# Performance work log

Measured on AMD Instinct MI355X. Metric: run time of the kernel, lower is better.

## Reference

```python
import jax, jax.numpy as jnp
import numpy as np

NQ, M, ND, N, H, DIM = 32, 32, 200, 160, 768, 128
TEMP = 0.1      # log_softmax temperature
TAU = 0.5       # gumbel-softmax temperature
NEG = -10000.0


def _l2norm(x):
    # F.normalize(p=2, dim=-1) with eps clamp
    n = jnp.maximum(jnp.linalg.norm(x, axis=-1, keepdims=True), 1e-12)
    return x / n


def setup_inputs() -> dict:
    key = jax.random.key(0)
    k1, k2, k3, k4, k5, k6 = jax.random.split(key, 6)
    Q = jax.random.normal(k1, (NQ, M, H), dtype=jnp.float32)
    D = jax.random.normal(k2, (ND, N, H), dtype=jnp.float32)
    q_mask = jax.random.randint(k3, (NQ, M), 0, 2).astype(jnp.float32)
    d_mask = jax.random.randint(k4, (ND, N), 0, 2).astype(jnp.float32)
    # pre-sampled Gumbel(0,1) noise for gumbel_softmax (fixed for determinism)
    u = jax.random.uniform(k5, (NQ, ND, M, N), dtype=jnp.float32,
                           minval=1e-6, maxval=1.0 - 1e-6)
    gumbel_noise = -jnp.log(-jnp.log(u))
    # proj_linear: Linear(768, dim, bias=False)
    W_proj = jax.random.normal(k6, (H, DIM), dtype=jnp.float32) / np.sqrt(H)
    return {"Q": Q, "D": D, "q_mask": q_mask, "d_mask": d_mask,
            "gumbel_noise": gumbel_noise, "W_proj": W_proj}


def reference(Q, D, q_mask, d_mask, gumbel_noise, W_proj):
    # project + L2-normalize token embeddings
    Qp = _l2norm(Q @ W_proj)            # [q, m, dim]
    Dp = _l2norm(D @ W_proj)            # [d, n, dim]

    # pairwise token similarities: [q, d, m, n]
    sim = jnp.einsum('qmh,dnh->qdmn', Qp, Dp)

    dm = d_mask[None, :, None, :]       # [1, d, 1, n]
    sim_masked = sim * dm + (1.0 - dm) * NEG

    logits = jax.nn.log_softmax(sim_masked / TEMP, axis=-1)

    # gumbel_softmax(tau=0.5, hard=True) with straight-through
    y_soft = jax.nn.softmax((logits + gumbel_noise) / TAU, axis=-1)
    idx = jnp.argmax(y_soft, axis=-1)
    y_hard = jax.nn.one_hot(idx, N, dtype=y_soft.dtype)
    y = jax.lax.stop_gradient(y_hard - y_soft) + y_soft

    # select doc token per query token, mask query tokens, sum -> [q, d]
    scores = (y * sim_masked).sum(-1)          # [q, d, m]
    scores = scores * q_mask[:, None, :]
    return scores.sum(-1)                      # [q, d]
```

## Files before the change

kernel.cpp:

```cpp
#include <hip/hip_runtime.h>
#include <math.h>

#define NQ_   32
#define M_    32
#define ND_   200
#define N_    160
#define H_    768
#define DIM_  128

__global__ __launch_bounds__(128) void proj_norm_row_kernel(
    const float* __restrict__ X, const float* __restrict__ W,
    float* __restrict__ Y)
{
    const int row = blockIdx.x;
    const int c   = threadIdx.x;
    const float* x = X + (size_t)row * H_;
    float acc = 0.0f;
#pragma unroll 8
    for (int h = 0; h < H_; ++h)
        acc = fmaf(x[h], W[(size_t)h * DIM_ + c], acc);

    float ss = __fmul_rn(acc, acc);
    ss = __fadd_rn(ss, __shfl_xor(ss, 1));
    ss = __fadd_rn(ss, __shfl_xor(ss, 2));
    ss = __fadd_rn(ss, __shfl_xor(ss, 4));
    ss = __fadd_rn(ss, __shfl_xor(ss, 8));
    ss = __fadd_rn(ss, __shfl_xor(ss, 16));
    ss = __fadd_rn(ss, __shfl_xor(ss, 32));
    __shared__ float sred[2];
    if ((c & 63) == 0) sred[c >> 6] = ss;
    __syncthreads();
    float tot = __fadd_rn(sred[0], sred[1]);
    float nrm = fmaxf(sqrtf(tot), 1e-12f);
    Y[(size_t)row * DIM_ + c] = acc / nrm;
}

__global__ __launch_bounds__(256) void proj_norm_tiled_kernel(
    const float* __restrict__ X, const float* __restrict__ W,
    float* __restrict__ Y)
{
    __shared__ float Xt[16][128];
    __shared__ float Ws[16][128];
    const int tid = threadIdx.x;
    const int rb  = blockIdx.x * 128;
    const int cg  = tid & 15;
    const int rg  = tid >> 4;

    float acc[8][8];
#pragma unroll
    for (int i = 0; i < 8; ++i)
#pragma unroll
        for (int j = 0; j < 8; ++j) acc[i][j] = 0.0f;

    for (int kc = 0; kc < H_; kc += 16) {
#pragma unroll
        for (int it = 0; it < 2; ++it) {
            int f = tid + it * 256;
            int row = f >> 2;
            int c4  = f & 3;
            float4 v = *reinterpret_cast<const float4*>(
                &X[(size_t)(rb + row) * H_ + kc + c4 * 4]);
            Xt[c4*4+0][row] = v.x;
            Xt[c4*4+1][row] = v.y;
            Xt[c4*4+2][row] = v.z;
            Xt[c4*4+3][row] = v.w;
        }
#pragma unroll
        for (int it = 0; it < 2; ++it) {
            int f = tid + it * 256;
            int wr = f >> 5;
            int wc = f & 31;
            float4 v = *reinterpret_cast<const float4*>(
                &W[(size_t)(kc + wr) * DIM_ + wc * 4]);
            *reinterpret_cast<float4*>(&Ws[wr][wc * 4]) = v;
        }
        __syncthreads();
#pragma unroll
        for (int k = 0; k < 16; ++k) {
            float a[8], b[8];
            *reinterpret_cast<float4*>(&a[0]) = *reinterpret_cast<const float4*>(&Xt[k][rg*8]);
            *reinterpret_cast<float4*>(&a[4]) = *reinterpret_cast<const float4*>(&Xt[k][rg*8+4]);
            *reinterpret_cast<float4*>(&b[0]) = *reinterpret_cast<const float4*>(&Ws[k][cg*8]);
            *reinterpret_cast<float4*>(&b[4]) = *reinterpret_cast<const float4*>(&Ws[k][cg*8+4]);
#pragma unroll
            for (int i = 0; i < 8; ++i)
#pragma unroll
                for (int j = 0; j < 8; ++j)
                    acc[i][j] = fmaf(a[i], b[j], acc[i][j]);
        }
        __syncthreads();
    }

#pragma unroll
    for (int i = 0; i < 8; ++i) {
        float ss = 0.0f;
#pragma unroll
        for (int j = 0; j < 8; ++j) ss = __fadd_rn(ss, __fmul_rn(acc[i][j], acc[i][j]));
        ss = __fadd_rn(ss, __shfl_xor(ss, 1));
        ss = __fadd_rn(ss, __shfl_xor(ss, 2));
        ss = __fadd_rn(ss, __shfl_xor(ss, 4));
        ss = __fadd_rn(ss, __shfl_xor(ss, 8));
        float nrm = fmaxf(sqrtf(ss), 1e-12f);
        float o[8];
#pragma unroll
        for (int j = 0; j < 8; ++j) o[j] = acc[i][j] / nrm;
        size_t base = (size_t)(rb + rg*8 + i) * DIM_ + cg*8;
        *reinterpret_cast<float4*>(&Y[base])     = *reinterpret_cast<float4*>(&o[0]);
        *reinterpret_cast<float4*>(&Y[base + 4]) = *reinterpret_cast<float4*>(&o[4]);
    }
}

__global__ __launch_bounds__(256) void score_kernel(
    const float* __restrict__ Qp, const float* __restrict__ Dp,
    const float* __restrict__ qmask, const float* __restrict__ dmask,
    const float* __restrict__ gum, float* __restrict__ out)
{
    __shared__ float Qt[16][32];
    __shared__ float Dt[4][16][164];
    const int tid  = threadIdx.x;
    const int w    = tid >> 6;
    const int lane = tid & 63;
    const int mg   = lane >> 4;
    const int ng   = lane & 15;
    const int q    = blockIdx.x & 31;
    const int db   = blockIdx.x >> 5;
    const int d    = db * 4 + w;

    const float* Qb = Qp + (size_t)q * M_ * DIM_;
    const float* Db = Dp + (size_t)d * N_ * DIM_;

    float acc[8][10];
#pragma unroll
    for (int i = 0; i < 8; ++i)
#pragma unroll
        for (int j = 0; j < 10; ++j) acc[i][j] = 0.0f;

    for (int kc = 0; kc < DIM_; kc += 16) {
        if (tid < 128) {
            int m = tid >> 2, c4 = tid & 3;
            float4 v = *reinterpret_cast<const float4*>(&Qb[(size_t)m * DIM_ + kc + c4*4]);
            Qt[c4*4+0][m] = v.x;
            Qt[c4*4+1][m] = v.y;
            Qt[c4*4+2][m] = v.z;
            Qt[c4*4+3][m] = v.w;
        }
#pragma unroll
        for (int it = 0; it < 10; ++it) {
            int f = lane + it * 64;
            int n = f >> 2, c4 = f & 3;
            float4 v = *reinterpret_cast<const float4*>(&Db[(size_t)n * DIM_ + kc + c4*4]);
            Dt[w][c4*4+0][n] = v.x;
            Dt[w][c4*4+1][n] = v.y;
            Dt[w][c4*4+2][n] = v.z;
            Dt[w][c4*4+3][n] = v.w;
        }
        __syncthreads();
#pragma unroll
        for (int k = 0; k < 16; ++k) {
            float a[8], b[10];
            *reinterpret_cast<float4*>(&a[0]) = *reinterpret_cast<const float4*>(&Qt[k][mg*8]);
            *reinterpret_cast<float4*>(&a[4]) = *reinterpret_cast<const float4*>(&Qt[k][mg*8+4]);
            const float* bp = &Dt[w][k][ng*10];
#pragma unroll
            for (int j2 = 0; j2 < 5; ++j2)
                *reinterpret_cast<float2*>(&b[j2*2]) = *reinterpret_cast<const float2*>(&bp[j2*2]);
#pragma unroll
            for (int i = 0; i < 8; ++i)
#pragma unroll
                for (int j = 0; j < 10; ++j)
                    acc[i][j] = fmaf(a[i], b[j], acc[i][j]);
        }
        __syncthreads();
    }

    float dmv[10];
#pragma unroll
    for (int j = 0; j < 10; ++j)
        dmv[j] = dmask[(size_t)d * N_ + ng*10 + j];

    const float* gq = gum + ((size_t)q * ND_ + d) * ((size_t)M_ * N_);

    float partial = 0.0f;
#pragma unroll
    for (int i = 0; i < 8; ++i) {
        const int m = mg*8 + i;
        float x[10];
        float mx = -3.402823466e38f;
#pragma unroll
        for (int j = 0; j < 10; ++j) {
            float sm = (dmv[j] != 0.0f) ? acc[i][j] : -10000.0f;
            x[j] = sm / 0.1f;
            mx = fmaxf(mx, x[j]);
        }
        mx = fmaxf(mx, __shfl_xor(mx, 1));
        mx = fmaxf(mx, __shfl_xor(mx, 2));
        mx = fmaxf(mx, __shfl_xor(mx, 4));
        mx = fmaxf(mx, __shfl_xor(mx, 8));

        float se = 0.0f;
#pragma unroll
        for (int j = 0; j < 10; ++j) se = __fadd_rn(se, expf(x[j] - mx));
        se = __fadd_rn(se, __shfl_xor(se, 1));
        se = __fadd_rn(se, __shfl_xor(se, 2));
        se = __fadd_rn(se, __shfl_xor(se, 4));
        se = __fadd_rn(se, __shfl_xor(se, 8));
        const float lse = logf(se);

        float g[10];
        const float2* gp = reinterpret_cast<const float2*>(&gq[(size_t)m * N_ + ng*10]);
#pragma unroll
        for (int j2 = 0; j2 < 5; ++j2)
            *reinterpret_cast<float2*>(&g[j2*2]) = gp[j2];

        float z[10];
        float mz = -3.402823466e38f;
#pragma unroll
        for (int j = 0; j < 10; ++j) {
            z[j] = ((x[j] - mx - lse) + g[j]) / 0.5f;
            mz = fmaxf(mz, z[j]);
        }
        mz = fmaxf(mz, __shfl_xor(mz, 1));
        mz = fmaxf(mz, __shfl_xor(mz, 2));
        mz = fmaxf(mz, __shfl_xor(mz, 4));
        mz = fmaxf(mz, __shfl_xor(mz, 8));

        float e2[10];
        float s2 = 0.0f;
#pragma unroll
        for (int j = 0; j < 10; ++j) { e2[j] = expf(z[j] - mz); s2 = __fadd_rn(s2, e2[j]); }
        s2 = __fadd_rn(s2, __shfl_xor(s2, 1));
        s2 = __fadd_rn(s2, __shfl_xor(s2, 2));
        s2 = __fadd_rn(s2, __shfl_xor(s2, 4));
        s2 = __fadd_rn(s2, __shfl_xor(s2, 8));

        float besty = -1.0f; int bestn = 0x7fffffff; float bests = 0.0f;
#pragma unroll
        for (int j = 0; j < 10; ++j) {
            float y = e2[j] / s2;
            if (y > besty) {
                besty = y;
                bestn = ng*10 + j;
                bests = (dmv[j] != 0.0f) ? acc[i][j] : -10000.0f;
            }
        }
#pragma unroll
        for (int dl = 1; dl < 16; dl <<= 1) {
            float oy = __shfl_xor(besty, dl);
            int   on = __shfl_xor(bestn, dl);
            float os = __shfl_xor(bests, dl);
            if (oy > besty || (oy == besty && on < bestn)) {
                besty = oy; bestn = on; bests = os;
            }
        }
        const float qmv = qmask[q * M_ + m];
        if (ng == 0) partial = __fadd_rn(partial, __fmul_rn(bests, qmv));
    }
    partial = __fadd_rn(partial, __shfl_xor(partial, 16));
    partial = __fadd_rn(partial, __shfl_xor(partial, 32));
    if (lane == 0) out[(size_t)q * ND_ + d] = partial;
}

extern "C" void kernel_launch(void* const* d_in, const int* in_sizes, int n_in,
                              void* d_out, int out_size, void* d_ws, size_t ws_size,
                              hipStream_t stream)
{
    const float* Q   = (const float*)d_in[0];
    const float* D   = (const float*)d_in[1];
    const float* qm  = (const float*)d_in[2];
    const float* dm  = (const float*)d_in[3];
    const float* gum = (const float*)d_in[4];
    const float* W   = (const float*)d_in[5];
    float* out = (float*)d_out;

    float* Qp = (float*)d_ws;
    float* Dp = Qp + (size_t)NQ_ * M_ * DIM_;

    proj_norm_row_kernel<<<dim3(NQ_ * M_), dim3(128), 0, stream>>>(Q, W, Qp);
    proj_norm_tiled_kernel<<<dim3((ND_ * N_) / 128), dim3(256), 0, stream>>>(D, W, Dp);
    score_kernel<<<dim3(NQ_ * (ND_ / 4)), dim3(256), 0, stream>>>(Qp, Dp, qm, dm, gum, out);
}
```

Before: 566.7 us.

## Merge Q/D projections, store transposed embeddings, use direct global-to-LDS loads in scoring

Fuses the Q and D projection kernels into one tiled kernel with 32-row tiles, which writes normalized embeddings transposed (dim-major per doc/query). The score kernel becomes one 64-thread block per (q,d) pair that loads contiguous transposed slices straight into LDS via global_load_lds. This removes the per-element transposes in the score kernel and one launch. The cost is strided uncoalesced stores in the projection and smaller blocks with a sync every 8 k-steps, which may limit latency hiding.

```diff
diff --git a/kernel.cpp b/kernel.cpp
--- a/kernel.cpp
+++ b/kernel.cpp
@@ -7,83 +7,62 @@
 #define N_    160
 #define H_    768
 #define DIM_  128
-
-__global__ __launch_bounds__(128) void proj_norm_row_kernel(
-    const float* __restrict__ X, const float* __restrict__ W,
-    float* __restrict__ Y)
+#define DROWS_ (ND_ * N_)
+#define QROWS_ (NQ_ * M_)
+#define TROWS_ (DROWS_ + QROWS_)
+
+__device__ __forceinline__ void gl_lds16(const float* g, float* l) {
+    __builtin_amdgcn_global_load_lds(
+        (const __attribute__((address_space(1))) unsigned int*)g,
+        (__attribute__((address_space(3))) unsigned int*)l, 16, 0, 0);
+}
+
+__global__ __launch_bounds__(128) void proj_kernel(
+    const float* __restrict__ Dmat, const float* __restrict__ Qmat,
+    const float* __restrict__ W, float* __restrict__ DpT,
+    float* __restrict__ QpT)
 {
-    const int row = blockIdx.x;
-    const int c   = threadIdx.x;
-    const float* x = X + (size_t)row * H_;
-    float acc = 0.0f;
-#pragma unroll 8
-    for (int h = 0; h < H_; ++h)
-        acc = fmaf(x[h], W[(size_t)h * DIM_ + c], acc);
-
-    float ss = __fmul_rn(acc, acc);
-    ss = __fadd_rn(ss, __shfl_xor(ss, 1));
-    ss = __fadd_rn(ss, __shfl_xor(ss, 2));
-    ss = __fadd_rn(ss, __shfl_xor(ss, 4));
-    ss = __fadd_rn(ss, __shfl_xor(ss, 8));
-    ss = __fadd_rn(ss, __shfl_xor(ss, 16));
-    ss = __fadd_rn(ss, __shfl_xor(ss, 32));
-    __shared__ float sred[2];
-    if ((c & 63) == 0) sred[c >> 6] = ss;
-    __syncthreads();
-    float tot = __fadd_rn(sred[0], sred[1]);
-    float nrm = fmaxf(sqrtf(tot), 1e-12f);
-    Y[(size_t)row * DIM_ + c] = acc / nrm;
-}
-
-__global__ __launch_bounds__(256) void proj_norm_tiled_kernel(
-    const float* __restrict__ X, const float* __restrict__ W,
-    float* __restrict__ Y)
-{
-    __shared__ float Xt[16][128];
+    __shared__ float Xt[16][32];
     __shared__ float Ws[16][128];
     const int tid = threadIdx.x;
-    const int rb  = blockIdx.x * 128;
+    const int rb  = blockIdx.x * 32;
     const int cg  = tid & 15;
     const int rg  = tid >> 4;
 
-    float acc[8][8];
-#pragma unroll
-    for (int i = 0; i < 8; ++i)
+    float acc[4][8];
+#pragma unroll
+    for (int i = 0; i < 4; ++i)
 #pragma unroll
         for (int j = 0; j < 8; ++j) acc[i][j] = 0.0f;
 
     for (int kc = 0; kc < H_; kc += 16) {
-#pragma unroll
-        for (int it = 0; it < 2; ++it) {
-            int f = tid + it * 256;
-            int row = f >> 2;
-            int c4  = f & 3;
-            float4 v = *reinterpret_cast<const float4*>(
-                &X[(size_t)(rb + row) * H_ + kc + c4 * 4]);
+        {
+            int row = tid >> 2, c4 = tid & 3;
+            int r = rb + row;
+            const float* xr = (r < DROWS_) ? (Dmat + (size_t)r * H_)
+                                           : (Qmat + (size_t)(r - DROWS_) * H_);
+            float4 v = *reinterpret_cast<const float4*>(xr + kc + c4 * 4);
             Xt[c4*4+0][row] = v.x;
             Xt[c4*4+1][row] = v.y;
             Xt[c4*4+2][row] = v.z;
             Xt[c4*4+3][row] = v.w;
         }
 #pragma unroll
-        for (int it = 0; it < 2; ++it) {
-            int f = tid + it * 256;
-            int wr = f >> 5;
-            int wc = f & 31;
-            float4 v = *reinterpret_cast<const float4*>(
-                &W[(size_t)(kc + wr) * DIM_ + wc * 4]);
-            *reinterpret_cast<float4*>(&Ws[wr][wc * 4]) = v;
+        for (int it = 0; it < 4; ++it) {
+            int f = tid + it * 128;
+            int wr = f >> 5, wc = f & 31;
+            *reinterpret_cast<float4*>(&Ws[wr][wc*4]) =
+                *reinterpret_cast<const float4*>(&W[(size_t)(kc + wr) * DIM_ + wc * 4]);
         }
         __syncthreads();
 #pragma unroll
         for (int k = 0; k < 16; ++k) {
-            float a[8], b[8];
-            *reinterpret_cast<float4*>(&a[0]) = *reinterpret_cast<const float4*>(&Xt[k][rg*8]);
-            *reinterpret_cast<float4*>(&a[4]) = *reinterpret_cast<const float4*>(&Xt[k][rg*8+4]);
+            float a[4], b[8];
+            *reinterpret_cast<float4*>(&a[0]) = *reinterpret_cast<const float4*>(&Xt[k][rg*4]);
             *reinterpret_cast<float4*>(&b[0]) = *reinterpret_cast<const float4*>(&Ws[k][cg*8]);
             *reinterpret_cast<float4*>(&b[4]) = *reinterpret_cast<const float4*>(&Ws[k][cg*8+4]);
 #pragma unroll
-            for (int i = 0; i < 8; ++i)
+            for (int i = 0; i < 4; ++i)
 #pragma unroll
                 for (int j = 0; j < 8; ++j)
                     acc[i][j] = fmaf(a[i], b[j], acc[i][j]);
@@ -92,7 +71,8 @@
     }
 
 #pragma unroll
-    for (int i = 0; i < 8; ++i) {
+    for (int i = 0; i < 4; ++i) {
+        int r = rb + rg * 4 + i;
         float ss = 0.0f;
 #pragma unroll
         for (int j = 0; j < 8; ++j) ss = __fadd_rn(ss, __fmul_rn(acc[i][j], acc[i][j]));
@@ -101,33 +81,38 @@
         ss = __fadd_rn(ss, __shfl_xor(ss, 4));
         ss = __fadd_rn(ss, __shfl_xor(ss, 8));
         float nrm = fmaxf(sqrtf(ss), 1e-12f);
-        float o[8];
-#pragma unroll
-        for (int j = 0; j < 8; ++j) o[j] = acc[i][j] / nrm;
-        size_t base = (size_t)(rb + rg*8 + i) * DIM_ + cg*8;
-        *reinterpret_cast<float4*>(&Y[base])     = *reinterpret_cast<float4*>(&o[0]);
-        *reinterpret_cast<float4*>(&Y[base + 4]) = *reinterpret_cast<float4*>(&o[4]);
-    }
-}
-
-__global__ __launch_bounds__(256) void score_kernel(
-    const float* __restrict__ Qp, const float* __restrict__ Dp,
+        if (r < DROWS_) {
+            int dd = r / 160, n = r - dd * 160;
+            float* o = DpT + (size_t)dd * (DIM_ * N_) + n;
+#pragma unroll
+            for (int j = 0; j < 8; ++j)
+                o[(size_t)(cg*8 + j) * N_] = acc[i][j] / nrm;
+        } else {
+            int rq = r - DROWS_;
+            int qq = rq >> 5, m = rq & 31;
+            float* o = QpT + (size_t)qq * (DIM_ * M_) + m;
+#pragma unroll
+            for (int j = 0; j < 8; ++j)
+                o[(size_t)(cg*8 + j) * M_] = acc[i][j] / nrm;
+        }
+    }
+}
+
+__global__ __launch_bounds__(64) void score_kernel(
+    const float* __restrict__ QpT, const float* __restrict__ DpT,
     const float* __restrict__ qmask, const float* __restrict__ dmask,
     const float* __restrict__ gum, float* __restrict__ out)
 {
-    __shared__ float Qt[16][32];
-    __shared__ float Dt[4][16][164];
-    const int tid  = threadIdx.x;
-    const int w    = tid >> 6;
-    const int lane = tid & 63;
+    __shared__ float Qt[8][32];
+    __shared__ float Dt[8][160];
+    const int lane = threadIdx.x;
     const int mg   = lane >> 4;
     const int ng   = lane & 15;
     const int q    = blockIdx.x & 31;
-    const int db   = blockIdx.x >> 5;
-    const int d    = db * 4 + w;
-
-    const float* Qb = Qp + (size_t)q * M_ * DIM_;
-    const float* Db = Dp + (size_t)d * N_ * DIM_;
+    const int d    = blockIdx.x >> 5;
+
+    const float* Qb = QpT + (size_t)q * (DIM_ * M_);
+    const float* Db = DpT + (size_t)d * (DIM_ * N_);
 
     float acc[8][10];
 #pragma unroll
@@ -135,32 +120,18 @@
 #pragma unroll
         for (int j = 0; j < 10; ++j) acc[i][j] = 0.0f;
 
-    for (int kc = 0; kc < DIM_; kc += 16) {
-        if (tid < 128) {
-            int m = tid >> 2, c4 = tid & 3;
-            float4 v = *reinterpret_cast<const float4*>(&Qb[(size_t)m * DIM_ + kc + c4*4]);
-            Qt[c4*4+0][m] = v.x;
-            Qt[c4*4+1][m] = v.y;
-            Qt[c4*4+2][m] = v.z;
-            Qt[c4*4+3][m] = v.w;
-        }
-#pragma unroll
-        for (int it = 0; it < 10; ++it) {
-            int f = lane + it * 64;
-            int n = f >> 2, c4 = f & 3;
-            float4 v = *reinterpret_cast<const float4*>(&Db[(size_t)n * DIM_ + kc + c4*4]);
-            Dt[w][c4*4+0][n] = v.x;
-            Dt[w][c4*4+1][n] = v.y;
-            Dt[w][c4*4+2][n] = v.z;
-            Dt[w][c4*4+3][n] = v.w;
-        }
-        __syncthreads();
-#pragma unroll
-        for (int k = 0; k < 16; ++k) {
+    for (int kc = 0; kc < DIM_; kc += 8) {
+        gl_lds16(Qb + kc * M_ + lane * 4, &Qt[0][0]);
+#pragma unroll
+        for (int c = 0; c < 5; ++c)
+            gl_lds16(Db + kc * N_ + c * 256 + lane * 4, &Dt[0][0] + c * 256);
+        __syncthreads();
+#pragma unroll
+        for (int k = 0; k < 8; ++k) {
             float a[8], b[10];
             *reinterpret_cast<float4*>(&a[0]) = *reinterpret_cast<const float4*>(&Qt[k][mg*8]);
             *reinterpret_cast<float4*>(&a[4]) = *reinterpret_cast<const float4*>(&Qt[k][mg*8+4]);
-            const float* bp = &Dt[w][k][ng*10];
+            const float* bp = &Dt[k][ng*10];
 #pragma unroll
             for (int j2 = 0; j2 < 5; ++j2)
                 *reinterpret_cast<float2*>(&b[j2*2]) = *reinterpret_cast<const float2*>(&bp[j2*2]);
@@ -272,10 +243,9 @@
     const float* W   = (const float*)d_in[5];
     float* out = (float*)d_out;
 
-    float* Qp = (float*)d_ws;
-    float* Dp = Qp + (size_t)NQ_ * M_ * DIM_;
-
-    proj_norm_row_kernel<<<dim3(NQ_ * M_), dim3(128), 0, stream>>>(Q, W, Qp);
-    proj_norm_tiled_kernel<<<dim3((ND_ * N_) / 128), dim3(256), 0, stream>>>(D, W, Dp);
-    score_kernel<<<dim3(NQ_ * (ND_ / 4)), dim3(256), 0, stream>>>(Qp, Dp, qm, dm, gum, out);
-}
+    float* QpT = (float*)d_ws;
+    float* DpT = QpT + (size_t)QROWS_ * DIM_;
+
+    proj_kernel<<<dim3(TROWS_ / 32), dim3(128), 0, stream>>>(D, Q, W, DpT, QpT);
+    score_kernel<<<dim3(NQ_ * ND_), dim3(64), 0, stream>>>(QpT, DpT, qm, dm, gum, out);
+}
```

Result: faster. 503.9 us (-11.1%).
